# Performance work log

Measured on AMD Instinct MI355X. Metric: run time of the kernel, lower is better.

## Reference

```python
import jax, jax.numpy as jnp
import numpy as np

B, S, E, H = 8, 2048, 1024, 64

def setup_inputs() -> dict:
    key = jax.random.key(0)
    k1, k2, k3, k4 = jax.random.split(key, 4)
    scale = 0.02
    return {
        "x": jax.random.normal(k1, (B, S, E), dtype=jnp.float32),
        "Wq": jax.random.normal(k2, (E, H), dtype=jnp.float32) * scale,
        "Wk": jax.random.normal(k3, (E, H), dtype=jnp.float32) * scale,
        "Wv": jax.random.normal(k4, (E, H), dtype=jnp.float32) * scale,
    }

def reference(x, Wq, Wk, Wv):
    # x: [B, S, E]; projections to [B, S, H]
    q = jnp.einsum("bse,eh->bsh", x, Wq)
    k = jnp.einsum("bse,eh->bsh", x, Wk)
    v = jnp.einsum("bse,eh->bsh", x, Wv)
    head_size = Wq.shape[1]
    # NOTE: original divides by head_size (not sqrt(head_size))
    scores = jnp.einsum("bqh,bkh->bqk", q, k) / head_size  # [B, S, S]
    seq = q.shape[1]
    causal = jnp.tril(jnp.ones((seq, seq), dtype=bool))
    scores = jnp.where(causal, scores, -jnp.inf)
    attn = jax.nn.softmax(scores, axis=-1)
    # dropout p=0.0 (eval) -> identity
    return jnp.einsum("bqk,bkh->bqh", attn, v)
```

## Files before the change

kernel.cpp:

```cpp
#include <hip/hip_runtime.h>


typedef __bf16 bf16;
typedef bf16 bf16x8 __attribute__((ext_vector_type(8)));
typedef bf16 bf16x4 __attribute__((ext_vector_type(4)));
typedef float v4f __attribute__((ext_vector_type(4)));

#define MFMA_BF16 __builtin_amdgcn_mfma_f32_16x16x32_bf16

constexpr int SEQ = 2048, EDIM = 1024, HDIM = 64;
constexpr float SCALE_L2E = 1.4426950408889634f / 64.0f;

__global__ __launch_bounds__(256) void prep_w_kernel(
    const float* __restrict__ Wq, const float* __restrict__ Wk,
    const float* __restrict__ Wv, bf16* __restrict__ Wt) {
  int mat = blockIdx.x >> 5, kseg = blockIdx.x & 31;
  const float* src = mat == 0 ? Wq : (mat == 1 ? Wk : Wv);
  int n = threadIdx.x & 63;
  int k0 = kseg * 32 + (threadIdx.x >> 6) * 8;
  bf16x8 v;
#pragma unroll
  for (int j = 0; j < 8; ++j)
    v[j] = (bf16)src[(k0 + j) * 64 + n];
  *reinterpret_cast<bf16x8*>(Wt + (size_t)(mat * 64 + n) * EDIM + k0) = v;
}

__global__ __launch_bounds__(256) void proj_kernel(
    const float* __restrict__ x, const bf16* __restrict__ Wt,
    bf16* __restrict__ qw, bf16* __restrict__ kw, bf16* __restrict__ vT) {
  __shared__ __align__(16) bf16 As[2][32][72];
  __shared__ __align__(16) bf16 Bs[2][192][72];

  const int t = threadIdx.x;
  const int m0 = blockIdx.x * 32;
  const int wv = t >> 6, lane = t & 63, quad = lane >> 4, l16 = lane & 15;

  v4f acc[2][3] = {};
  float4 aReg[2];
  bf16x8 bReg[6];

  auto loadA = [&](int kk) {
#pragma unroll
    for (int p = 0; p < 2; ++p) {
      int flat = p * 1024 + t * 4;
      int r = flat >> 6, c = flat & 63;
      aReg[p] = *reinterpret_cast<const float4*>(
          x + (size_t)(m0 + r) * EDIM + kk * 64 + c);
    }
  };
  auto loadB = [&](int kk) {
#pragma unroll
    for (int p = 0; p < 6; ++p) {
      int idx = p * 256 + t;
      int r = idx >> 3, off = (idx & 7) * 8;
      bReg[p] = *reinterpret_cast<const bf16x8*>(
          Wt + (size_t)r * EDIM + kk * 64 + off);
    }
  };

  loadA(0);
  loadB(0);

  for (int kk = 0; kk < 16; ++kk) {
    const int buf = kk & 1;
#pragma unroll
    for (int p = 0; p < 2; ++p) {
      int flat = p * 1024 + t * 4;
      int r = flat >> 6, c = flat & 63;
      bf16x4 h4 = {(bf16)aReg[p].x, (bf16)aReg[p].y,
                   (bf16)aReg[p].z, (bf16)aReg[p].w};
      *reinterpret_cast<bf16x4*>(&As[buf][r][c]) = h4;
    }
#pragma unroll
    for (int p = 0; p < 6; ++p) {
      int idx = p * 256 + t;
      int r = idx >> 3, off = (idx & 7) * 8;
      *reinterpret_cast<bf16x8*>(&Bs[buf][r][off]) = bReg[p];
    }
    __syncthreads();
    if (kk < 15) {
      loadA(kk + 1);
      loadB(kk + 1);
    }
#pragma unroll
    for (int ks = 0; ks < 2; ++ks) {
      bf16x8 af[2], bfr[3];
#pragma unroll
      for (int mi = 0; mi < 2; ++mi)
        af[mi] = *reinterpret_cast<const bf16x8*>(
            &As[buf][16 * mi + l16][32 * ks + 8 * quad]);
#pragma unroll
      for (int ni = 0; ni < 3; ++ni)
        bfr[ni] = *reinterpret_cast<const bf16x8*>(
            &Bs[buf][48 * wv + 16 * ni + l16][32 * ks + 8 * quad]);
#pragma unroll
      for (int mi = 0; mi < 2; ++mi)
#pragma unroll
        for (int ni = 0; ni < 3; ++ni)
          acc[mi][ni] = MFMA_BF16(af[mi], bfr[ni], acc[mi][ni], 0, 0, 0);
    }
  }

#pragma unroll
  for (int mi = 0; mi < 2; ++mi) {
    const int token0 = m0 + 16 * mi + 4 * quad;
#pragma unroll
    for (int ni = 0; ni < 3; ++ni) {
      int n = 48 * wv + 16 * ni + l16;
      if (n < 64) {
#pragma unroll
        for (int r = 0; r < 4; ++r)
          qw[(size_t)(token0 + r) * HDIM + n] = (bf16)acc[mi][ni][r];
      } else if (n < 128) {
#pragma unroll
        for (int r = 0; r < 4; ++r)
          kw[(size_t)(token0 + r) * HDIM + (n - 64)] = (bf16)acc[mi][ni][r];
      } else {
        int b = token0 >> 11, s0 = token0 & 2047;
        bf16x4 pk = {(bf16)acc[mi][ni][0], (bf16)acc[mi][ni][1],
                     (bf16)acc[mi][ni][2], (bf16)acc[mi][ni][3]};
        *reinterpret_cast<bf16x4*>(
            vT + ((size_t)(b * 64 + (n - 128))) * SEQ + s0) = pk;
      }
    }
  }
}

__global__ __launch_bounds__(256) void attn_kernel(
    const bf16* __restrict__ qw, const bf16* __restrict__ kw,
    const bf16* __restrict__ vT, float* __restrict__ out) {
  const int batch = blockIdx.x & 7;
  const int pi = blockIdx.x >> 3;
  const int w = threadIdx.x >> 6;
  const int lane = threadIdx.x & 63;
  const int quad = lane >> 4, l16 = lane & 15;

  __shared__ __align__(16) bf16 p_lds[4][2][32][68];
  __shared__ __align__(16) float o_lds[3][32][68];
  __shared__ float l_lds[3][32];

  const bf16* qB = qw + (size_t)batch * SEQ * HDIM;
  const bf16* kB = kw + (size_t)batch * SEQ * HDIM;
  const bf16* vB = vT + (size_t)batch * HDIM * SEQ;

  for (int sp = 0; sp < 2; ++sp) {
    const int j = sp ? (63 - pi) : pi;
    const int q0 = 32 * j;
    const int T64 = (j + 2) >> 1;
    const int nw = (T64 > w) ? (((T64 - 1 - w) >> 2) + 1) : 0;

    bf16x8 aq[2][2];
#pragma unroll
    for (int mi = 0; mi < 2; ++mi)
#pragma unroll
      for (int kf = 0; kf < 2; ++kf)
        aq[mi][kf] = *reinterpret_cast<const bf16x8*>(
            qB + (size_t)(q0 + 16 * mi + l16) * HDIM + 32 * kf + 8 * quad);

    v4f accO[2][4] = {};
    float l_part[2][4] = {{0.f, 0.f, 0.f, 0.f}, {0.f, 0.f, 0.f, 0.f}};
    bf16x8 kfr[4][2];

    auto loadK = [&](int jt) {
#pragma unroll
      for (int nt = 0; nt < 4; ++nt)
#pragma unroll
        for (int kf = 0; kf < 2; ++kf)
          kfr[nt][kf] = *reinterpret_cast<const bf16x8*>(
              kB + (size_t)(64 * jt + 16 * nt + l16) * HDIM + 32 * kf +
              8 * quad);
    };
    auto qk_exp_stage = [&](int jt, int slot) {
      v4f s[2][4] = {};
#pragma unroll
      for (int mi = 0; mi < 2; ++mi)
#pragma unroll
        for (int nt = 0; nt < 4; ++nt) {
          s[mi][nt] = MFMA_BF16(aq[mi][0], kfr[nt][0], s[mi][nt], 0, 0, 0);
          s[mi][nt] = MFMA_BF16(aq[mi][1], kfr[nt][1], s[mi][nt], 0, 0, 0);
        }
      const bool last = (jt == T64 - 1);
#pragma unroll
      for (int mi = 0; mi < 2; ++mi)
#pragma unroll
        for (int nt = 0; nt < 4; ++nt)
#pragma unroll
          for (int r = 0; r < 4; ++r) {
            float p = __builtin_amdgcn_exp2f(s[mi][nt][r] * SCALE_L2E);
            if (last &&
                (64 * jt + 16 * nt + l16 > q0 + 16 * mi + 4 * quad + r))
              p = 0.f;
            l_part[mi][r] += p;
            p_lds[w][slot][16 * mi + 4 * quad + r][16 * nt + l16] = (bf16)p;
          }
    };

    if (nw > 0) {
      loadK(w);
      qk_exp_stage(w, 0);
    }
    for (int i = 0; i < nw; ++i) {
      const int jt = w + 4 * i;
      const int k0 = 64 * jt;
      if (i + 1 < nw) loadK(jt + 4);
      bf16x8 vfr[4][2];
#pragma unroll
      for (int nt = 0; nt < 4; ++nt)
#pragma unroll
        for (int kc = 0; kc < 2; ++kc)
          vfr[nt][kc] = *reinterpret_cast<const bf16x8*>(
              vB + (size_t)(16 * nt + l16) * SEQ + k0 + 32 * kc + 8 * quad);
      asm volatile("s_waitcnt lgkmcnt(0)" ::: "memory");
      bf16x8 pa[2][2];
#pragma unroll
      for (int mi = 0; mi < 2; ++mi)
#pragma unroll
        for (int kc = 0; kc < 2; ++kc)
          pa[mi][kc] = *reinterpret_cast<const bf16x8*>(
              &p_lds[w][i & 1][16 * mi + l16][32 * kc + 8 * quad]);
      if (i + 1 < nw) qk_exp_stage(jt + 4, (i + 1) & 1);
#pragma unroll
      for (int mi = 0; mi < 2; ++mi)
#pragma unroll
        for (int nt = 0; nt < 4; ++nt) {
          accO[mi][nt] = MFMA_BF16(pa[mi][0], vfr[nt][0], accO[mi][nt], 0, 0, 0);
          accO[mi][nt] = MFMA_BF16(pa[mi][1], vfr[nt][1], accO[mi][nt], 0, 0, 0);
        }
    }

#pragma unroll
    for (int mi = 0; mi < 2; ++mi)
#pragma unroll
      for (int r = 0; r < 4; ++r) {
        float s = l_part[mi][r];
        s += __shfl_xor(s, 1, 16);
        s += __shfl_xor(s, 2, 16);
        s += __shfl_xor(s, 4, 16);
        s += __shfl_xor(s, 8, 16);
        l_part[mi][r] = s;
      }

    __syncthreads();
    if (w > 0) {
#pragma unroll
      for (int mi = 0; mi < 2; ++mi)
#pragma unroll
        for (int nt = 0; nt < 4; ++nt)
#pragma unroll
          for (int r = 0; r < 4; ++r)
            o_lds[w - 1][16 * mi + 4 * quad + r][16 * nt + l16] =
                accO[mi][nt][r];
      if (l16 == 0) {
#pragma unroll
        for (int mi = 0; mi < 2; ++mi)
#pragma unroll
          for (int r = 0; r < 4; ++r)
            l_lds[w - 1][16 * mi + 4 * quad + r] = l_part[mi][r];
      }
    }
    __syncthreads();
    if (w == 0) {
#pragma unroll
      for (int mi = 0; mi < 2; ++mi)
#pragma unroll
        for (int r = 0; r < 4; ++r) {
          const int row = 16 * mi + 4 * quad + r;
          float lt = l_part[mi][r] + l_lds[0][row] + l_lds[1][row] +
                     l_lds[2][row];
          float inv = 1.0f / lt;
          float* op = out + ((size_t)batch * SEQ + q0 + row) * HDIM;
#pragma unroll
          for (int nt = 0; nt < 4; ++nt)
            op[16 * nt + l16] =
                (accO[mi][nt][r] + o_lds[0][row][16 * nt + l16] +
                 o_lds[1][row][16 * nt + l16] +
                 o_lds[2][row][16 * nt + l16]) *
                inv;
        }
    }
  }
}

extern "C" void kernel_launch(void* const* d_in, const int* in_sizes, int n_in,
                              void* d_out, int out_size, void* d_ws,
                              size_t ws_size, hipStream_t stream) {
  const float* x = (const float*)d_in[0];
  const float* Wq = (const float*)d_in[1];
  const float* Wk = (const float*)d_in[2];
  const float* Wv = (const float*)d_in[3];

  char* ws = (char*)d_ws;
  bf16* Wt = (bf16*)(ws);
  bf16* qw = (bf16*)(ws + 0x60000);
  bf16* kw = (bf16*)(ws + 0x260000);
  bf16* vT = (bf16*)(ws + 0x460000);

  prep_w_kernel<<<96, 256, 0, stream>>>(Wq, Wk, Wv, Wt);
  proj_kernel<<<512, 256, 0, stream>>>(x, Wt, qw, kw, vT);
  attn_kernel<<<256, 256, 0, stream>>>(qw, kw, vT, (float*)d_out);
}
```

Measured before the change: 136.4 us.

## Load projection MFMA fragments directly from global memory, removing LDS staging

The projection kernel no longer stages x and W tiles through shared memory with block-wide barriers. Each wave now loads its own A and B MFMA fragments directly into registers, double-buffered two k-steps ahead, and computes a 16x96 output slice. This removes LDS writes, reads and __syncthreads. The trade-off is less coalesced, strided global accesses, duplicate reads across waves, and higher register pressure.

```diff
diff --git a/kernel.cpp b/kernel.cpp
--- a/kernel.cpp
+++ b/kernel.cpp
@@ -28,100 +28,82 @@
 __global__ __launch_bounds__(256) void proj_kernel(
     const float* __restrict__ x, const bf16* __restrict__ Wt,
     bf16* __restrict__ qw, bf16* __restrict__ kw, bf16* __restrict__ vT) {
-  __shared__ __align__(16) bf16 As[2][32][72];
-  __shared__ __align__(16) bf16 Bs[2][192][72];
-
   const int t = threadIdx.x;
+  const int w = t >> 6, lane = t & 63, quad = lane >> 4, l16 = lane & 15;
+  const int mi = w & 1, nh = w >> 1;
   const int m0 = blockIdx.x * 32;
-  const int wv = t >> 6, lane = t & 63, quad = lane >> 4, l16 = lane & 15;
-
-  v4f acc[2][3] = {};
-  float4 aReg[2];
-  bf16x8 bReg[6];
-
-  auto loadA = [&](int kk) {
-#pragma unroll
-    for (int p = 0; p < 2; ++p) {
-      int flat = p * 1024 + t * 4;
-      int r = flat >> 6, c = flat & 63;
-      aReg[p] = *reinterpret_cast<const float4*>(
-          x + (size_t)(m0 + r) * EDIM + kk * 64 + c);
-    }
+  const int row = m0 + 16 * mi + l16;
+
+  const float* xr = x + (size_t)row * EDIM + 8 * quad;
+  const bf16* wB = Wt + (size_t)(96 * nh + l16) * EDIM + 8 * quad;
+
+  v4f acc[6] = {};
+  float4 aA[2][4];
+  bf16x8 bReg[2][12];
+
+  auto loadA = [&](int kk, int slot) {
+    const float* p = xr + kk * 64;
+    aA[slot][0] = *reinterpret_cast<const float4*>(p);
+    aA[slot][1] = *reinterpret_cast<const float4*>(p + 4);
+    aA[slot][2] = *reinterpret_cast<const float4*>(p + 32);
+    aA[slot][3] = *reinterpret_cast<const float4*>(p + 36);
   };
-  auto loadB = [&](int kk) {
-#pragma unroll
-    for (int p = 0; p < 6; ++p) {
-      int idx = p * 256 + t;
-      int r = idx >> 3, off = (idx & 7) * 8;
-      bReg[p] = *reinterpret_cast<const bf16x8*>(
-          Wt + (size_t)r * EDIM + kk * 64 + off);
-    }
+  auto loadB = [&](int kk, int slot) {
+#pragma unroll
+    for (int nt = 0; nt < 6; ++nt)
+#pragma unroll
+      for (int ks = 0; ks < 2; ++ks)
+        bReg[slot][2 * nt + ks] = *reinterpret_cast<const bf16x8*>(
+            wB + (size_t)(16 * nt) * EDIM + kk * 64 + 32 * ks);
   };
 
-  loadA(0);
-  loadB(0);
-
+  loadA(0, 0);
+  loadB(0, 0);
+  loadA(1, 1);
+  loadB(1, 1);
+
+#pragma unroll 2
   for (int kk = 0; kk < 16; ++kk) {
     const int buf = kk & 1;
-#pragma unroll
-    for (int p = 0; p < 2; ++p) {
-      int flat = p * 1024 + t * 4;
-      int r = flat >> 6, c = flat & 63;
-      bf16x4 h4 = {(bf16)aReg[p].x, (bf16)aReg[p].y,
-                   (bf16)aReg[p].z, (bf16)aReg[p].w};
-      *reinterpret_cast<bf16x4*>(&As[buf][r][c]) = h4;
-    }
-#pragma unroll
-    for (int p = 0; p < 6; ++p) {
-      int idx = p * 256 + t;
-      int r = idx >> 3, off = (idx & 7) * 8;
-      *reinterpret_cast<bf16x8*>(&Bs[buf][r][off]) = bReg[p];
-    }
-    __syncthreads();
-    if (kk < 15) {
-      loadA(kk + 1);
-      loadB(kk + 1);
-    }
+    bf16x8 af[2];
 #pragma unroll
     for (int ks = 0; ks < 2; ++ks) {
-      bf16x8 af[2], bfr[3];
-#pragma unroll
-      for (int mi = 0; mi < 2; ++mi)
-        af[mi] = *reinterpret_cast<const bf16x8*>(
-            &As[buf][16 * mi + l16][32 * ks + 8 * quad]);
-#pragma unroll
-      for (int ni = 0; ni < 3; ++ni)
-        bfr[ni] = *reinterpret_cast<const bf16x8*>(
-            &Bs[buf][48 * wv + 16 * ni + l16][32 * ks + 8 * quad]);
-#pragma unroll
-      for (int mi = 0; mi < 2; ++mi)
-#pragma unroll
-        for (int ni = 0; ni < 3; ++ni)
-          acc[mi][ni] = MFMA_BF16(af[mi], bfr[ni], acc[mi][ni], 0, 0, 0);
-    }
+      float4 lo = aA[buf][2 * ks], hi = aA[buf][2 * ks + 1];
+      af[ks][0] = (bf16)lo.x; af[ks][1] = (bf16)lo.y;
+      af[ks][2] = (bf16)lo.z; af[ks][3] = (bf16)lo.w;
+      af[ks][4] = (bf16)hi.x; af[ks][5] = (bf16)hi.y;
+      af[ks][6] = (bf16)hi.z; af[ks][7] = (bf16)hi.w;
+    }
+    if (kk + 2 < 16) loadA(kk + 2, buf);
+#pragma unroll
+    for (int nt = 0; nt < 6; ++nt)
+#pragma unroll
+      for (int ks = 0; ks < 2; ++ks)
+        acc[nt] = MFMA_BF16(af[ks], bReg[buf][2 * nt + ks], acc[nt], 0, 0, 0);
+    if (kk + 2 < 16) loadB(kk + 2, buf);
   }
 
-#pragma unroll
-  for (int mi = 0; mi < 2; ++mi) {
-    const int token0 = m0 + 16 * mi + 4 * quad;
-#pragma unroll
-    for (int ni = 0; ni < 3; ++ni) {
-      int n = 48 * wv + 16 * ni + l16;
-      if (n < 64) {
-#pragma unroll
-        for (int r = 0; r < 4; ++r)
-          qw[(size_t)(token0 + r) * HDIM + n] = (bf16)acc[mi][ni][r];
-      } else if (n < 128) {
-#pragma unroll
-        for (int r = 0; r < 4; ++r)
-          kw[(size_t)(token0 + r) * HDIM + (n - 64)] = (bf16)acc[mi][ni][r];
-      } else {
-        int b = token0 >> 11, s0 = token0 & 2047;
-        bf16x4 pk = {(bf16)acc[mi][ni][0], (bf16)acc[mi][ni][1],
-                     (bf16)acc[mi][ni][2], (bf16)acc[mi][ni][3]};
-        *reinterpret_cast<bf16x4*>(
-            vT + ((size_t)(b * 64 + (n - 128))) * SEQ + s0) = pk;
-      }
+  const int token0 = m0 + 16 * mi + 4 * quad;
+#pragma unroll
+  for (int nt = 0; nt < 6; ++nt) {
+    const int tl = 6 * nh + nt;
+    if (tl < 4) {
+      const int n = 16 * tl + l16;
+#pragma unroll
+      for (int r = 0; r < 4; ++r)
+        qw[(size_t)(token0 + r) * HDIM + n] = (bf16)acc[nt][r];
+    } else if (tl < 8) {
+      const int n = 16 * (tl - 4) + l16;
+#pragma unroll
+      for (int r = 0; r < 4; ++r)
+        kw[(size_t)(token0 + r) * HDIM + n] = (bf16)acc[nt][r];
+    } else {
+      const int hrow = 16 * (tl - 8) + l16;
+      const int b = token0 >> 11, s0 = token0 & 2047;
+      bf16x4 pk = {(bf16)acc[nt][0], (bf16)acc[nt][1], (bf16)acc[nt][2],
+                   (bf16)acc[nt][3]};
+      *reinterpret_cast<bf16x4*>(vT + ((size_t)(b * 64 + hrow)) * SEQ + s0) =
+          pk;
     }
   }
 }
```

After: 168.0 us. 1.23x slower.
